# Kernel optimization log

Hardware: AMD Instinct MI355X
Metric: run time of the kernel (lower is better)

Reference implementation:

```python
import jax, jax.numpy as jnp
import numpy as np

D_MODEL = 1024
N_HEADS = 16
D_K = D_MODEL // N_HEADS
ROPE_THETA = 10000.0


def setup_inputs() -> dict:
    key = jax.random.key(0)
    ks = jax.random.split(key, 5)
    B, S = 2, 2048
    std = (2.0 / (D_MODEL + D_MODEL)) ** 0.5
    x = jax.random.normal(ks[0], (B, S, D_MODEL), dtype=jnp.float32)
    Wq = jax.random.normal(ks[1], (D_MODEL, D_MODEL), dtype=jnp.float32) * std
    Wk = jax.random.normal(ks[2], (D_MODEL, D_MODEL), dtype=jnp.float32) * std
    Wv = jax.random.normal(ks[3], (D_MODEL, D_MODEL), dtype=jnp.float32) * std
    Wo = jax.random.normal(ks[4], (D_MODEL, D_MODEL), dtype=jnp.float32) * std
    token_positions = jnp.arange(S, dtype=jnp.int64 if jax.config.jax_enable_x64 else jnp.int32)
    return {"x": x, "Wq": Wq, "Wk": Wk, "Wv": Wv, "Wo": Wo,
            "token_positions": token_positions}


def _apply_rope(t, token_positions):
    # t: [B, H, S, d_k]; token_positions: [S]
    inv_freq = 1.0 / (ROPE_THETA ** (jnp.arange(0, D_K, 2, dtype=jnp.float32) / D_K))  # [d_k/2]
    freqs = token_positions.astype(jnp.float32)[:, None] * inv_freq[None, :]  # [S, d_k/2]
    cos, sin = jnp.cos(freqs), jnp.sin(freqs)
    x1, x2 = t[..., ::2], t[..., 1::2]
    xr = x1 * cos - x2 * sin
    yr = x1 * sin + x2 * cos
    # interleave back to even/odd positions
    out = jnp.stack([xr, yr], axis=-1).reshape(t.shape)
    return out


def reference(x, Wq, Wk, Wv, Wo, token_positions):
    B, S, D = x.shape
    H, dk = N_HEADS, D_K
    # projections: weight is [d_out, d_in], applied as x @ W.T
    def proj_heads(W):
        y = jnp.einsum('bsd,ed->bse', x, W)
        return y.reshape(B, S, H, dk).transpose(0, 2, 1, 3)  # [B,H,S,dk]
    q = proj_heads(Wq)
    k = proj_heads(Wk)
    v = proj_heads(Wv)
    q = _apply_rope(q, token_positions)
    k = _apply_rope(k, token_positions)
    scores = jnp.einsum('bhqd,bhkd->bhqk', q, k) / jnp.sqrt(jnp.float32(dk))
    causal = jnp.tril(jnp.ones((S, S), dtype=bool))
    scores = jnp.where(causal, scores, -jnp.inf)
    attn = jax.nn.softmax(scores, axis=-1)
    out = jnp.einsum('bhqk,bhkd->bhqd', attn, v)  # [B,H,S,dk]
    out = out.transpose(0, 2, 1, 3).reshape(B, S, D)
    return jnp.einsum('bsd,ed->bse', out, Wo)
```

## Files before the change

### kernel.cpp

```cpp
#include <hip/hip_runtime.h>

typedef __bf16 bf16x8 __attribute__((ext_vector_type(8)));
typedef float f32x4 __attribute__((ext_vector_type(4)));
typedef unsigned short u16x8 __attribute__((ext_vector_type(8)));


__device__ __forceinline__ unsigned short f2bf(float f) {
  unsigned u = __builtin_bit_cast(unsigned, f);
  u = (u + 0x7FFFu + ((u >> 16) & 1u)) >> 16;
  return (unsigned short)u;
}

__device__ __forceinline__ unsigned cvt_pk_bf16(float lo, float hi) {
  unsigned r;
  asm("v_cvt_pk_bf16_f32 %0, %1, %2" : "=v"(r) : "v"(lo), "v"(hi));
  return r;
}

__device__ __forceinline__ void load_lds16(const void* g, void* l) {
  __builtin_amdgcn_global_load_lds(
      (__attribute__((address_space(1))) void*)g,
      (__attribute__((address_space(3))) void*)l, 16, 0, 0);
}

__global__ __launch_bounds__(256) void k_convert(
    const float* __restrict__ x,
    const float* __restrict__ wq, const float* __restrict__ wk,
    const float* __restrict__ wv, const float* __restrict__ wo,
    unsigned short* __restrict__ xb,
    unsigned short* __restrict__ wqb, unsigned short* __restrict__ wkb,
    unsigned short* __restrict__ wvb, unsigned short* __restrict__ wob) {
  const int g = blockIdx.x * 256 + threadIdx.x;
  const float* src;
  unsigned short* dst;
  int off;
  if (g < (1 << 20)) {
    src = x; dst = xb; off = g;
  } else {
    const int q = g - (1 << 20);
    const int t = q >> 18;
    off = q & ((1 << 18) - 1);
    src = (t == 0) ? wq : (t == 1) ? wk : (t == 2) ? wv : wo;
    dst = (t == 0) ? wqb : (t == 1) ? wkb : (t == 2) ? wvb : wob;
  }
  const float4 v = ((const float4*)src)[off];
  ushort4 r;
  r.x = f2bf(v.x); r.y = f2bf(v.y); r.z = f2bf(v.z); r.w = f2bf(v.w);
  ((ushort4*)dst)[off] = r;
}

__global__ __launch_bounds__(256) void k_rope_tab(const int* __restrict__ tpos,
                                                  float* __restrict__ ct,
                                                  float* __restrict__ st) {
  const int idx = blockIdx.x * 256 + threadIdx.x;
  const int s = idx >> 5, i = idx & 31;
  const double p = (double)tpos[s];
  const double f = p * pow(10000.0, -(double)(2 * i) / 64.0);
  ct[idx] = (float)cos(f);
  st[idx] = (float)sin(f);
}

__device__ __forceinline__ void gemm_core_1024(
    const unsigned short* __restrict__ Ag,
    const unsigned short* __restrict__ Bg,
    unsigned short* As, unsigned short* Bs, f32x4 (&acc)[4][4], int tid) {
  const int lane = tid & 63;
  const int w = tid >> 6;
  const int wm = (w >> 1) * 64;
  const int wn = (w & 1) * 64;
  const int lr = lane & 15;
  const int lg8 = (lane >> 4) * 8;
  const int c0 = tid, c1 = 256 + tid;
  const int ar0 = c0 >> 2, ac0 = (c0 & 3) * 8;
  const int ar1 = c1 >> 2, ac1 = (c1 & 3) * 8;

  auto stage = [&](int buf, int kt) {
    unsigned short* Ab = As + buf * 4096;
    unsigned short* Bb = Bs + buf * 4096;
    load_lds16(Ag + ar0 * 1024 + kt + ac0, Ab + c0 * 8);
    load_lds16(Ag + ar1 * 1024 + kt + ac1, Ab + c1 * 8);
    load_lds16(Bg + ar0 * 1024 + kt + ac0, Bb + c0 * 8);
    load_lds16(Bg + ar1 * 1024 + kt + ac1, Bb + c1 * 8);
  };

  stage(0, 0);
  stage(1, 32);
  int cur = 0;
  for (int ki = 0; ki < 32; ++ki) {
    if (ki + 2 < 32) {
      int nb = cur + 2; if (nb >= 3) nb -= 3;
      stage(nb, (ki + 2) * 32);
      asm volatile("s_waitcnt vmcnt(8)" ::: "memory");
    } else if (ki + 1 < 32) {
      asm volatile("s_waitcnt vmcnt(4)" ::: "memory");
    } else {
      asm volatile("s_waitcnt vmcnt(0)" ::: "memory");
    }
    __builtin_amdgcn_s_barrier();
    const unsigned short* Ab = As + cur * 4096;
    const unsigned short* Bb = Bs + cur * 4096;
    bf16x8 af[4], bfv[4];
#pragma unroll
    for (int mi = 0; mi < 4; ++mi)
      af[mi] = *(const bf16x8*)(Ab + (wm + mi * 16 + lr) * 32 + lg8);
#pragma unroll
    for (int ni = 0; ni < 4; ++ni)
      bfv[ni] = *(const bf16x8*)(Bb + (wn + ni * 16 + lr) * 32 + lg8);
    __builtin_amdgcn_s_setprio(1);
#pragma unroll
    for (int mi = 0; mi < 4; ++mi)
#pragma unroll
      for (int ni = 0; ni < 4; ++ni)
        acc[mi][ni] = __builtin_amdgcn_mfma_f32_16x16x32_bf16(
            af[mi], bfv[ni], acc[mi][ni], 0, 0, 0);
    __builtin_amdgcn_s_setprio(0);
    __builtin_amdgcn_s_barrier();
    ++cur; if (cur == 3) cur = 0;
  }
}

__device__ __forceinline__ void gemm_core_bm64(
    const unsigned short* __restrict__ Ag,
    const unsigned short* __restrict__ Bg,
    unsigned short* As, unsigned short* Bs, f32x4 (&acc)[2][4], int tid) {
  const int lane = tid & 63;
  const int w = tid >> 6;
  const int wm = (w >> 1) * 32;
  const int wn = (w & 1) * 64;
  const int lr = lane & 15;
  const int lg8 = (lane >> 4) * 8;
  const int ar = tid >> 2, ac = (tid & 3) * 8;
  const int c0 = tid, c1 = 256 + tid;
  const int br0 = c0 >> 2, bc0 = (c0 & 3) * 8;
  const int br1 = c1 >> 2, bc1 = (c1 & 3) * 8;

  auto stage = [&](int buf, int kt) {
    load_lds16(Ag + ar * 1024 + kt + ac, As + buf * 2048 + tid * 8);
    load_lds16(Bg + br0 * 1024 + kt + bc0, Bs + buf * 4096 + c0 * 8);
    load_lds16(Bg + br1 * 1024 + kt + bc1, Bs + buf * 4096 + c1 * 8);
  };

  stage(0, 0);
  stage(1, 32);
  int cur = 0;
  for (int ki = 0; ki < 32; ++ki) {
    if (ki + 2 < 32) {
      int nb = cur + 2; if (nb >= 3) nb -= 3;
      stage(nb, (ki + 2) * 32);
      asm volatile("s_waitcnt vmcnt(6)" ::: "memory");
    } else if (ki + 1 < 32) {
      asm volatile("s_waitcnt vmcnt(3)" ::: "memory");
    } else {
      asm volatile("s_waitcnt vmcnt(0)" ::: "memory");
    }
    __builtin_amdgcn_s_barrier();
    const unsigned short* Ab = As + cur * 2048;
    const unsigned short* Bb = Bs + cur * 4096;
    bf16x8 af[2], bfv[4];
#pragma unroll
    for (int mi = 0; mi < 2; ++mi)
      af[mi] = *(const bf16x8*)(Ab + (wm + mi * 16 + lr) * 32 + lg8);
#pragma unroll
    for (int ni = 0; ni < 4; ++ni)
      bfv[ni] = *(const bf16x8*)(Bb + (wn + ni * 16 + lr) * 32 + lg8);
    __builtin_amdgcn_s_setprio(1);
#pragma unroll
    for (int mi = 0; mi < 2; ++mi)
#pragma unroll
      for (int ni = 0; ni < 4; ++ni)
        acc[mi][ni] = __builtin_amdgcn_mfma_f32_16x16x32_bf16(
            af[mi], bfv[ni], acc[mi][ni], 0, 0, 0);
    __builtin_amdgcn_s_setprio(0);
    __builtin_amdgcn_s_barrier();
    ++cur; if (cur == 3) cur = 0;
  }
}

__global__ __launch_bounds__(256) void k_proj(
    const unsigned short* __restrict__ Xb,
    const unsigned short* __restrict__ Wq, const unsigned short* __restrict__ Wk,
    const unsigned short* __restrict__ Wv,
    const float* __restrict__ ctab, const float* __restrict__ stab,
    unsigned short* __restrict__ Qo, unsigned short* __restrict__ Ko,
    unsigned short* __restrict__ Vo) {
  __shared__ __align__(16) unsigned short As[3 * 128 * 32];
  __shared__ __align__(16) unsigned short Bs[3 * 128 * 32];
  const int z = blockIdx.z;
  const unsigned short* Wsel = (z == 0) ? Wq : (z == 1) ? Wk : Wv;
  unsigned short* Out = (z == 0) ? Qo : (z == 1) ? Ko : Vo;
  const int tid = threadIdx.x;
  const int bm = blockIdx.x * 128, bn = blockIdx.y * 128;
  f32x4 acc[4][4] = {};
  gemm_core_1024(Xb + (size_t)bm * 1024, Wsel + (size_t)bn * 1024, As, Bs, acc, tid);

  const int lane = tid & 63, w = tid >> 6;
  const int wm = (w >> 1) * 64, wn = (w & 1) * 64;
  const int lr = lane & 15, lg = lane >> 4;

  if (z == 2) {
#pragma unroll
    for (int mi = 0; mi < 4; ++mi) {
      const int r0 = bm + wm + mi * 16 + lg * 4;
      const int s = r0 & 2047, b = r0 >> 11;
#pragma unroll
      for (int ni = 0; ni < 4; ++ni) {
        const int e = bn + wn + ni * 16 + lr;
        const int h = e >> 6, d = e & 63;
        ushort4 pk;
        pk.x = f2bf(acc[mi][ni][0]);
        pk.y = f2bf(acc[mi][ni][1]);
        pk.z = f2bf(acc[mi][ni][2]);
        pk.w = f2bf(acc[mi][ni][3]);
        *(ushort4*)&Out[((size_t)(b * 16 + h) * 64 + d) * 2048 + s] = pk;
      }
    }
    return;
  }

  const bool odd = lane & 1;
#pragma unroll
  for (int mi = 0; mi < 4; ++mi) {
#pragma unroll
    for (int ni = 0; ni < 4; ++ni) {
#pragma unroll
      for (int reg = 0; reg < 4; ++reg) {
        const int r = bm + wm + mi * 16 + lg * 4 + reg;
        const int e = bn + wn + ni * 16 + lr;
        float val = acc[mi][ni][reg];
        const float partner = __shfl_xor(val, 1);
        const int s = r & 2047, b = r >> 11;
        const int h = e >> 6, d = e & 63;
        const int i = d >> 1;
        const float c = ctab[s * 32 + i];
        const float sn = stab[s * 32 + i];
        const float outv = odd ? (val * c + partner * sn) : (val * c - partner * sn);
        Out[((size_t)(b * 16 + h) * 2048 + s) * 64 + d] = f2bf(outv);
      }
    }
  }
}

__global__ __launch_bounds__(64, 2) void k_attn(
    const unsigned short* __restrict__ Q, const unsigned short* __restrict__ K,
    const unsigned short* __restrict__ Vt, unsigned short* __restrict__ O) {
  __shared__ __align__(16) unsigned short Vs[2][64 * 64];
  __shared__ __align__(16) unsigned short Pl[16 * 68];
  const int L = blockIdx.x;
  const int bh = (L & 7) * 4 + ((L >> 3) & 3);
  const int p = L >> 5;
  const int qrowA = p * 16, qrowB = (127 - p) * 16;
  const int Ta = (qrowA + 79) >> 6;
  const int Tb = (qrowB + 79) >> 6;
  const int lane = threadIdx.x & 63;
  const int lr = lane & 15, lg = lane >> 4;
  const unsigned short* Qg = Q + (size_t)bh * 2048 * 64;
  const unsigned short* Kg = K + (size_t)bh * 2048 * 64;
  const unsigned short* Vg = Vt + (size_t)bh * 64 * 2048;

  bf16x8 qfA[2], qfB[2];
#pragma unroll
  for (int h = 0; h < 2; ++h) {
    qfA[h] = *(const bf16x8*)(Qg + (qrowA + lr) * 64 + h * 32 + lg * 8);
    qfB[h] = *(const bf16x8*)(Qg + (qrowB + lr) * 64 + h * 32 + lg * 8);
  }

  u16x8 ouv;
#pragma unroll
  for (int j = 0; j < 8; ++j) ouv[j] = 0x3F80;
  const bf16x8 onesf = __builtin_bit_cast(bf16x8, ouv);

  f32x4 oA[4] = {}, oB[4] = {};
  f32x4 lAa = {}, lBa = {};
  float mA = -__builtin_inff(), mB = -__builtin_inff();

  const float SCL = 0.125f * 1.44269504088896f;
  const float THR = 8.0f;

  const int kbase = lr * 64 + lg * 8;
  const int vbase = (lane >> 3) * 2048 + (((lane & 7) ^ (lane >> 3)) * 8);

  auto loadK = [&](bf16x8 (&kd)[4][2], int kv) {
    const unsigned short* base = Kg + (size_t)kv * 4096 + kbase;
#pragma unroll
    for (int nt = 0; nt < 4; ++nt)
#pragma unroll
      for (int h = 0; h < 2; ++h)
        kd[nt][h] = *(const bf16x8*)(base + nt * 1024 + h * 32);
  };
  auto issueV = [&](int buf, int kv) {
    const unsigned short* src = Vg + kv * 64 + vbase;
    unsigned short* dst = &Vs[buf][0] + lane * 8;
#pragma unroll
    for (int i0 = 0; i0 < 8; ++i0)
      load_lds16(src + i0 * 16384, dst + i0 * 512);
  };

  auto soft = [&](f32x4 (&s)[4], float& m, f32x4& la, f32x4 (&oacc)[4],
                  int qrow, bool needmask, int kv) {
    if (needmask) {
      const int qg = qrow + lr;
#pragma unroll
      for (int nt = 0; nt < 4; ++nt)
#pragma unroll
        for (int reg = 0; reg < 4; ++reg) {
          const int kg = kv * 64 + nt * 16 + lg * 4 + reg;
          if (kg > qg) s[nt][reg] = -__builtin_inff();
        }
    }
    float t0 = fmaxf(fmaxf(s[0][0], s[0][1]), fmaxf(s[0][2], s[0][3]));
    float t1 = fmaxf(fmaxf(s[1][0], s[1][1]), fmaxf(s[1][2], s[1][3]));
    float t2 = fmaxf(fmaxf(s[2][0], s[2][1]), fmaxf(s[2][2], s[2][3]));
    float t3 = fmaxf(fmaxf(s[3][0], s[3][1]), fmaxf(s[3][2], s[3][3]));
    float pm = fmaxf(fmaxf(t0, t1), fmaxf(t2, t3));
    if (!__all(pm <= m + THR)) {
      pm = fmaxf(pm, __shfl_xor(pm, 16));
      pm = fmaxf(pm, __shfl_xor(pm, 32));
      if (__any(pm > m)) {
        const float mn = fmaxf(m, pm);
        const float al = exp2f(SCL * (m - mn));
        m = mn;
#pragma unroll
        for (int reg = 0; reg < 4; ++reg) la[reg] *= al;
#pragma unroll
        for (int nt = 0; nt < 4; ++nt)
#pragma unroll
          for (int reg = 0; reg < 4; ++reg) oacc[nt][reg] *= al;
      }
    }
    const float msc = SCL * m;
    unsigned short* prow = Pl + lr * 68;
#pragma unroll
    for (int nt = 0; nt < 4; ++nt) {
      const float p0 = exp2f(s[nt][0] * SCL - msc);
      const float p1 = exp2f(s[nt][1] * SCL - msc);
      const float p2 = exp2f(s[nt][2] * SCL - msc);
      const float p3 = exp2f(s[nt][3] * SCL - msc);
      const unsigned w01 = cvt_pk_bf16(p0, p1);
      const unsigned w23 = cvt_pk_bf16(p2, p3);
      ushort4 pk;
      pk.x = (unsigned short)w01; pk.y = (unsigned short)(w01 >> 16);
      pk.z = (unsigned short)w23; pk.w = (unsigned short)(w23 >> 16);
      *(ushort4*)(prow + nt * 16 + lg * 4) = pk;
    }
  };

  bf16x8 kbufA[4][2], kbufB[4][2];
  loadK(kbufA, 0);
  issueV(0, 0);

  auto iter = [&](int t, bf16x8 (&kc)[4][2], bf16x8 (&kn)[4][2]) {
    const bool more = (t + 1 < Tb);
    const bool actA = (t < Ta);
    if (more) { loadK(kn, t + 1); issueV((t + 1) & 1, t + 1); }

    f32x4 sB[4], sA[4];
    __builtin_amdgcn_s_setprio(1);
#pragma unroll
    for (int nt = 0; nt < 4; ++nt) {
      f32x4 z = {0.f, 0.f, 0.f, 0.f};
      z = __builtin_amdgcn_mfma_f32_16x16x32_bf16(kc[nt][0], qfB[0], z, 0, 0, 0);
      sB[nt] = __builtin_amdgcn_mfma_f32_16x16x32_bf16(kc[nt][1], qfB[1], z, 0, 0, 0);
    }
    if (actA)
#pragma unroll
      for (int nt = 0; nt < 4; ++nt) {
        f32x4 z = {0.f, 0.f, 0.f, 0.f};
        z = __builtin_amdgcn_mfma_f32_16x16x32_bf16(kc[nt][0], qfA[0], z, 0, 0, 0);
        sA[nt] = __builtin_amdgcn_mfma_f32_16x16x32_bf16(kc[nt][1], qfA[1], z, 0, 0, 0);
      }
    __builtin_amdgcn_s_setprio(0);

    soft(sB, mB, lBa, oB, qrowB, t == Tb - 1, t);
    bf16x8 paB[2], paA[2];
#pragma unroll
    for (int ks = 0; ks < 2; ++ks)
      paB[ks] = *(const bf16x8*)(Pl + lr * 68 + ks * 32 + lg * 8);
    if (actA) {
      soft(sA, mA, lAa, oA, qrowA, t == Ta - 1, t);
#pragma unroll
      for (int ks = 0; ks < 2; ++ks)
        paA[ks] = *(const bf16x8*)(Pl + lr * 68 + ks * 32 + lg * 8);
    }

    if (more) asm volatile("s_waitcnt vmcnt(16)" ::: "memory");
    else      asm volatile("s_waitcnt vmcnt(0)" ::: "memory");

    const unsigned short* Vw = &Vs[t & 1][0];
    __builtin_amdgcn_s_setprio(1);
    lBa = __builtin_amdgcn_mfma_f32_16x16x32_bf16(onesf, paB[0], lBa, 0, 0, 0);
    lBa = __builtin_amdgcn_mfma_f32_16x16x32_bf16(onesf, paB[1], lBa, 0, 0, 0);
    if (actA) {
      lAa = __builtin_amdgcn_mfma_f32_16x16x32_bf16(onesf, paA[0], lAa, 0, 0, 0);
      lAa = __builtin_amdgcn_mfma_f32_16x16x32_bf16(onesf, paA[1], lAa, 0, 0, 0);
    }
#pragma unroll
    for (int nt = 0; nt < 4; ++nt) {
      const int row = nt * 16 + lr;
      const bf16x8 vb0 = *(const bf16x8*)(Vw + row * 64 + ((lg ^ (row & 7)) * 8));
      const bf16x8 vb1 = *(const bf16x8*)(Vw + row * 64 + (((lg + 4) ^ (row & 7)) * 8));
      oB[nt] = __builtin_amdgcn_mfma_f32_16x16x32_bf16(vb0, paB[0], oB[nt], 0, 0, 0);
      oB[nt] = __builtin_amdgcn_mfma_f32_16x16x32_bf16(vb1, paB[1], oB[nt], 0, 0, 0);
      if (actA) {
        oA[nt] = __builtin_amdgcn_mfma_f32_16x16x32_bf16(vb0, paA[0], oA[nt], 0, 0, 0);
        oA[nt] = __builtin_amdgcn_mfma_f32_16x16x32_bf16(vb1, paA[1], oA[nt], 0, 0, 0);
      }
    }
    __builtin_amdgcn_s_setprio(0);
  };

  int t = 0;
  for (;;) {
    iter(t, kbufA, kbufB); ++t; if (t >= Tb) break;
    iter(t, kbufB, kbufA); ++t; if (t >= Tb) break;
  }

  const int b = bh >> 4, h = bh & 15;
  auto wrO = [&](f32x4 (&oacc)[4], float l, int qrow) {
    const float inv = 1.0f / l;
    unsigned short* dst = &O[((size_t)b * 2048 + qrow + lr) * 1024 + h * 64];
#pragma unroll
    for (int nt = 0; nt < 4; ++nt) {
      const unsigned w01 = cvt_pk_bf16(oacc[nt][0] * inv, oacc[nt][1] * inv);
      const unsigned w23 = cvt_pk_bf16(oacc[nt][2] * inv, oacc[nt][3] * inv);
      ushort4 pk;
      pk.x = (unsigned short)w01; pk.y = (unsigned short)(w01 >> 16);
      pk.z = (unsigned short)w23; pk.w = (unsigned short)(w23 >> 16);
      *(ushort4*)(dst + nt * 16 + lg * 4) = pk;
    }
  };
  wrO(oA, lAa[0], qrowA);
  wrO(oB, lBa[0], qrowB);
}

__global__ __launch_bounds__(256) void k_out(const unsigned short* __restrict__ Ab,
                                             const unsigned short* __restrict__ Wo,
                                             float* __restrict__ Out) {
  __shared__ __align__(16) unsigned short As[3 * 64 * 32];
  __shared__ __align__(16) unsigned short Bs[3 * 128 * 32];
  const int tid = threadIdx.x;
  const int bm = blockIdx.x * 64, bn = blockIdx.y * 128;
  f32x4 acc[2][4] = {};
  gemm_core_bm64(Ab + (size_t)bm * 1024, Wo + (size_t)bn * 1024, As, Bs, acc, tid);
  const int lane = tid & 63, w = tid >> 6;
  const int wm = (w >> 1) * 32, wn = (w & 1) * 64;
  const int lr = lane & 15, lg = lane >> 4;
#pragma unroll
  for (int mi = 0; mi < 2; ++mi)
#pragma unroll
    for (int ni = 0; ni < 4; ++ni)
#pragma unroll
      for (int reg = 0; reg < 4; ++reg) {
        const int r = bm + wm + mi * 16 + lg * 4 + reg;
        const int e = bn + wn + ni * 16 + lr;
        Out[(size_t)r * 1024 + e] = acc[mi][ni][reg];
      }
}

extern "C" void kernel_launch(void* const* d_in, const int* in_sizes, int n_in,
                              void* d_out, int out_size, void* d_ws, size_t ws_size,
                              hipStream_t stream) {
  const float* x = (const float*)d_in[0];
  const float* Wq = (const float*)d_in[1];
  const float* Wk = (const float*)d_in[2];
  const float* Wv = (const float*)d_in[3];
  const float* Wo = (const float*)d_in[4];
  const int* tpos = (const int*)d_in[5];
  float* out = (float*)d_out;
  char* ws = (char*)d_ws;
  const size_t MB = 1024 * 1024;
  unsigned short* xb = (unsigned short*)(ws);
  unsigned short* wqb = (unsigned short*)(ws + 8 * MB);
  unsigned short* wkb = (unsigned short*)(ws + 10 * MB);
  unsigned short* wvb = (unsigned short*)(ws + 12 * MB);
  unsigned short* wob = (unsigned short*)(ws + 14 * MB);
  unsigned short* Qb = (unsigned short*)(ws + 16 * MB);
  unsigned short* Kb = (unsigned short*)(ws + 24 * MB);
  unsigned short* Vtb = (unsigned short*)(ws + 32 * MB);
  unsigned short* Ab = (unsigned short*)(ws + 40 * MB);
  float* ctab = (float*)(ws + 48 * MB);
  float* stab = (float*)(ws + 48 * MB + 256 * 1024);

  k_convert<<<dim3(8192), dim3(256), 0, stream>>>(x, Wq, Wk, Wv, Wo, xb, wqb, wkb,
                                                  wvb, wob);
  k_rope_tab<<<dim3(256), dim3(256), 0, stream>>>(tpos, ctab, stab);
  k_proj<<<dim3(32, 8, 3), dim3(256), 0, stream>>>(xb, wqb, wkb, wvb, ctab, stab,
                                                   Qb, Kb, Vtb);
  k_attn<<<dim3(2048), dim3(64), 0, stream>>>(Qb, Kb, Vtb, Ab);
  k_out<<<dim3(64, 8), dim3(256), 0, stream>>>(Ab, wob, out);
}
```

Measured before the change: 151.6 us.

## Deepen K/V prefetch to two tiles ahead with triple-buffered K registers

Restructures the attention main loop to process KV tiles in pairs, using three rotating K register buffers so K is loaded two tiles ahead, and V tiles for t+2/t+3 are issued into the LDS double buffer after the previous PV consumes them. QK^T for the two query blocks is now computed and softmaxed sequentially, reusing a single score array to reduce register pressure. Waitcnt thresholds are adjusted to the deeper in-flight load count. The aim is to hide more global memory latency, at the cost of more VGPRs for K buffers and more complex vmcnt bookkeeping that could be wrong for odd tile counts.

Measured after the change: 295.1 us. 1.95x slower.

```diff
diff --git a/kernel.cpp b/kernel.cpp
--- a/kernel.cpp
+++ b/kernel.cpp
@@ -295,6 +295,17 @@
       load_lds16(src + i0 * 16384, dst + i0 * 512);
   };
 
+  auto qkt = [&](bf16x8 (&kc)[4][2], bf16x8 (&qf)[2], f32x4 (&s)[4]) {
+    __builtin_amdgcn_s_setprio(1);
+#pragma unroll
+    for (int nt = 0; nt < 4; ++nt) {
+      f32x4 z = {0.f, 0.f, 0.f, 0.f};
+      z = __builtin_amdgcn_mfma_f32_16x16x32_bf16(kc[nt][0], qf[0], z, 0, 0, 0);
+      s[nt] = __builtin_amdgcn_mfma_f32_16x16x32_bf16(kc[nt][1], qf[1], z, 0, 0, 0);
+    }
+    __builtin_amdgcn_s_setprio(0);
+  };
+
   auto soft = [&](f32x4 (&s)[4], float& m, f32x4& la, f32x4 (&oacc)[4],
                   int qrow, bool needmask, int kv) {
     if (needmask) {
@@ -344,48 +355,14 @@
     }
   };
 
-  bf16x8 kbufA[4][2], kbufB[4][2];
-  loadK(kbufA, 0);
-  issueV(0, 0);
-
-  auto iter = [&](int t, bf16x8 (&kc)[4][2], bf16x8 (&kn)[4][2]) {
-    const bool more = (t + 1 < Tb);
-    const bool actA = (t < Ta);
-    if (more) { loadK(kn, t + 1); issueV((t + 1) & 1, t + 1); }
-
-    f32x4 sB[4], sA[4];
-    __builtin_amdgcn_s_setprio(1);
-#pragma unroll
-    for (int nt = 0; nt < 4; ++nt) {
-      f32x4 z = {0.f, 0.f, 0.f, 0.f};
-      z = __builtin_amdgcn_mfma_f32_16x16x32_bf16(kc[nt][0], qfB[0], z, 0, 0, 0);
-      sB[nt] = __builtin_amdgcn_mfma_f32_16x16x32_bf16(kc[nt][1], qfB[1], z, 0, 0, 0);
-    }
-    if (actA)
-#pragma unroll
-      for (int nt = 0; nt < 4; ++nt) {
-        f32x4 z = {0.f, 0.f, 0.f, 0.f};
-        z = __builtin_amdgcn_mfma_f32_16x16x32_bf16(kc[nt][0], qfA[0], z, 0, 0, 0);
-        sA[nt] = __builtin_amdgcn_mfma_f32_16x16x32_bf16(kc[nt][1], qfA[1], z, 0, 0, 0);
-      }
-    __builtin_amdgcn_s_setprio(0);
-
-    soft(sB, mB, lBa, oB, qrowB, t == Tb - 1, t);
-    bf16x8 paB[2], paA[2];
+  auto readPa = [&](bf16x8 (&pa)[2]) {
 #pragma unroll
     for (int ks = 0; ks < 2; ++ks)
-      paB[ks] = *(const bf16x8*)(Pl + lr * 68 + ks * 32 + lg * 8);
-    if (actA) {
-      soft(sA, mA, lAa, oA, qrowA, t == Ta - 1, t);
-#pragma unroll
-      for (int ks = 0; ks < 2; ++ks)
-        paA[ks] = *(const bf16x8*)(Pl + lr * 68 + ks * 32 + lg * 8);
-    }
-
-    if (more) asm volatile("s_waitcnt vmcnt(16)" ::: "memory");
-    else      asm volatile("s_waitcnt vmcnt(0)" ::: "memory");
-
-    const unsigned short* Vw = &Vs[t & 1][0];
+      pa[ks] = *(const bf16x8*)(Pl + lr * 68 + ks * 32 + lg * 8);
+  };
+
+  auto pv = [&](int vbuf, bf16x8 (&paB)[2], bf16x8 (&paA)[2], bool actA) {
+    const unsigned short* Vw = &Vs[vbuf][0];
     __builtin_amdgcn_s_setprio(1);
     lBa = __builtin_amdgcn_mfma_f32_16x16x32_bf16(onesf, paB[0], lBa, 0, 0, 0);
     lBa = __builtin_amdgcn_mfma_f32_16x16x32_bf16(onesf, paB[1], lBa, 0, 0, 0);
@@ -408,10 +385,75 @@
     __builtin_amdgcn_s_setprio(0);
   };
 
-  int t = 0;
-  for (;;) {
-    iter(t, kbufA, kbufB); ++t; if (t >= Tb) break;
-    iter(t, kbufB, kbufA); ++t; if (t >= Tb) break;
+  bf16x8 kX[4][2], kY[4][2], kZ[4][2];
+
+  auto pairIter = [&](int t, bf16x8 (&c0)[4][2], bf16x8 (&c1)[4][2],
+                      bf16x8 (&nx)[4][2]) {
+    const bool actA0 = (t < Ta), actA1 = (t + 1 < Ta);
+    const bool haveK2 = (t + 2 < Tb), haveK3 = (t + 3 < Tb);
+    if (haveK2) loadK(nx, t + 2);
+
+    f32x4 s[4];
+    bf16x8 paB[2], paA[2];
+    qkt(c0, qfB, s);
+    soft(s, mB, lBa, oB, qrowB, t == Tb - 1, t);
+    readPa(paB);
+    if (actA0) {
+      qkt(c0, qfA, s);
+      soft(s, mA, lAa, oA, qrowA, t == Ta - 1, t);
+      readPa(paA);
+    }
+    if (haveK3) loadK(c0, t + 3);
+    if (haveK3)      asm volatile("s_waitcnt vmcnt(24)" ::: "memory");
+    else if (haveK2) asm volatile("s_waitcnt vmcnt(16)" ::: "memory");
+    else             asm volatile("s_waitcnt vmcnt(8)" ::: "memory");
+    pv(0, paB, paA, actA0);
+    asm volatile("s_waitcnt lgkmcnt(0)" ::: "memory");
+    if (haveK2) issueV(0, t + 2);
+
+    qkt(c1, qfB, s);
+    soft(s, mB, lBa, oB, qrowB, t + 1 == Tb - 1, t + 1);
+    readPa(paB);
+    if (actA1) {
+      qkt(c1, qfA, s);
+      soft(s, mA, lAa, oA, qrowA, t + 1 == Ta - 1, t + 1);
+      readPa(paA);
+    }
+    if (haveK3)      asm volatile("s_waitcnt vmcnt(24)" ::: "memory");
+    else if (haveK2) asm volatile("s_waitcnt vmcnt(16)" ::: "memory");
+    else             asm volatile("s_waitcnt vmcnt(0)" ::: "memory");
+    pv(1, paB, paA, actA1);
+    asm volatile("s_waitcnt lgkmcnt(0)" ::: "memory");
+    if (haveK3) issueV(1, t + 3);
+  };
+
+  auto singleIter = [&](int t, bf16x8 (&kc)[4][2]) {
+    f32x4 s[4];
+    bf16x8 paB[2];
+    qkt(kc, qfB, s);
+    soft(s, mB, lBa, oB, qrowB, true, t);
+    readPa(paB);
+    asm volatile("s_waitcnt vmcnt(0)" ::: "memory");
+    pv(t & 1, paB, paB, false);
+  };
+
+  loadK(kX, 0);
+  loadK(kY, 1);
+  issueV(0, 0);
+  issueV(1, 1);
+
+  int t = 0, rot = 0;
+  while (t + 1 < Tb) {
+    if (rot == 0)      pairIter(t, kX, kY, kZ);
+    else if (rot == 1) pairIter(t, kZ, kX, kY);
+    else               pairIter(t, kY, kZ, kX);
+    t += 2;
+    ++rot; if (rot == 3) rot = 0;
+  }
+  if (t < Tb) {
+    if (rot == 1)      singleIter(t, kZ);
+    else if (rot == 2) singleIter(t, kY);
+    else               singleIter(t, kX);
   }
 
   const int b = bh >> 4, h = bh & 15;
```
